# Kernel tuning notes

Measured on AMD Instinct MI355X. Metric: run time of the kernel, lower is better.

The kernel has to match this reference:

```python
import jax, jax.numpy as jnp
import numpy as np

SEQ_LEN, BATCH, TAGS = 512, 1024, 32
START_IDX, END_IDX = 30, 31
NEG = -10000.0


def setup_inputs() -> dict:
    key = jax.random.key(0)
    k1, k2 = jax.random.split(key)
    feats = jax.random.normal(k1, (SEQ_LEN, BATCH, TAGS), dtype=jnp.float32)
    mask = jnp.ones((SEQ_LEN, BATCH), dtype=jnp.float32)
    # xavier-normal-ish transition, then apply START/END constraints as in reset_parameters
    transition = jax.random.normal(k2, (TAGS, TAGS), dtype=jnp.float32) * (2.0 / (TAGS + TAGS)) ** 0.5
    transition = transition.at[START_IDX, :].set(NEG)
    transition = transition.at[:, END_IDX].set(NEG)
    return {"feats": feats, "mask": mask, "transition": transition}


def reference(feats, mask, transition):
    # feats: (T, N, M), mask: (T, N), transition: (M, M)
    batch_size, tag_size = feats.shape[1], feats.shape[2]
    alpha0 = jnp.full((batch_size, tag_size), NEG, dtype=feats.dtype)
    alpha0 = alpha0.at[:, START_IDX].set(0.0)

    def step(alpha, inp):
        feat_t, mask_t = inp  # (N, M), (N,)
        # score[n, j, i] = alpha[n, i] + transition[j, i] + feat[n, j]
        score = alpha[:, None, :] + transition[None, :, :] + feat_t[:, :, None]
        new_alpha = jax.nn.logsumexp(score, axis=-1)  # (N, M)
        m = mask_t[:, None]
        alpha = new_alpha * m + alpha * (1.0 - m)
        return alpha, None

    alpha, _ = jax.lax.scan(step, alpha0, (feats, mask))
    alpha = alpha + transition[END_IDX][None, :]
    return jax.nn.logsumexp(alpha, axis=-1)  # (N,)
```

## Files before the change

### kernel.cpp

```cpp
#include <hip/hip_runtime.h>


constexpr int SEQ = 512, BATCH = 1024, TAGS = 32;
constexpr int NC = 8, L = SEQ / NC;
constexpr int RROW = 16;

#define LOG2E 1.4426950408889634f
#define LN2   0.6931471805599453f

typedef __attribute__((ext_vector_type(8))) short short8;
typedef __attribute__((ext_vector_type(4))) float float4v;
typedef __attribute__((ext_vector_type(4))) unsigned uint4v;
union Frag8 { unsigned u[4]; short8 v; };

__device__ __forceinline__ unsigned pk_rn(float x, float y) {
  return __builtin_amdgcn_perm(__float_as_uint(y) + 0x8000u,
                               __float_as_uint(x) + 0x8000u, 0x07060302u);
}
__device__ __forceinline__ unsigned pk_tr(float x, float y) {
  return __builtin_amdgcn_perm(__float_as_uint(y), __float_as_uint(x), 0x07060302u);
}

extern "C" __global__ void __launch_bounds__(512, 6) crf_fused(
    const float* __restrict__ feats, const float* __restrict__ mask,
    const float* __restrict__ trans, float* __restrict__ out) {
  __shared__ unsigned gst[NC][66 * RROW];
  __shared__ float c2s[NC];
  __shared__ __align__(16) float ws[TAGS];
  __shared__ float c2x;

  const int wid = __builtin_amdgcn_readfirstlane((int)(threadIdx.x >> 6));
  const int lane = threadIdx.x & 63;
  const int b = blockIdx.x;
  const int s = lane & 15, q = lane >> 4;
  unsigned* Wp = &gst[wid][0];

  unsigned long long mb;
  {
    const float* fro = feats + ((size_t)(wid * L + lane) * BATCH + b) * TAGS;
    float4v fv[8];
#pragma unroll
    for (int i = 0; i < 8; ++i) fv[i] = *(const float4v*)(fro + 4 * i);
    const float mv = mask[(size_t)(wid * L + lane) * BATCH + b];
    mb = __ballot(mv != 0.0f);
    unsigned* rp = Wp + lane * RROW;
#pragma unroll
    for (int g = 0; g < 4; ++g) {
      uint4v t;
#pragma unroll
      for (int k2 = 0; k2 < 4; ++k2) {
        const int j = 4 * g + k2;
        const float lo = __builtin_amdgcn_exp2f(fv[j >> 2][j & 3] * LOG2E);
        const float hi = __builtin_amdgcn_exp2f(fv[4 + (j >> 2)][j & 3] * LOG2E);
        t[k2] = pk_rn(lo, hi);
      }
      *(uint4v*)(rp + 4 * g) = t;
    }
  }

  int sig[8];
#pragma unroll
  for (int i = 0; i < 8; ++i) sig[i] = (i < 4) ? (4 * q + i) : (16 + 4 * q + (i - 4));
  Frag8 e0, e1;
#pragma unroll
  for (int p = 0; p < 4; ++p) {
    e0.u[p] = pk_rn(__builtin_amdgcn_exp2f(trans[s * TAGS + sig[2 * p]] * LOG2E),
                    __builtin_amdgcn_exp2f(trans[s * TAGS + sig[2 * p + 1]] * LOG2E));
    e1.u[p] = pk_rn(__builtin_amdgcn_exp2f(trans[(16 + s) * TAGS + sig[2 * p]] * LOG2E),
                    __builtin_amdgcn_exp2f(trans[(16 + s) * TAGS + sig[2 * p + 1]] * LOG2E));
  }

  float4v P00 = {0, 0, 0, 0}, P01 = {0, 0, 0, 0}, P10 = {0, 0, 0, 0}, P11 = {0, 0, 0, 0};
#pragma unroll
  for (int p = 0; p < 4; ++p) {
    float one = (4 * q + p == s) ? 1.f : 0.f;
    P00[p] = one; P11[p] = one;
  }
  Frag8 B0, B1;
  float c2 = 0.f;
  const float4v zerov = {0.f, 0.f, 0.f, 0.f};

#define PACK_B()                                                        \
  { B0.u[0] = pk_tr(P00[0], P00[1]); B0.u[1] = pk_tr(P00[2], P00[3]);   \
    B0.u[2] = pk_tr(P10[0], P10[1]); B0.u[3] = pk_tr(P10[2], P10[3]);   \
    B1.u[0] = pk_tr(P01[0], P01[1]); B1.u[1] = pk_tr(P01[2], P01[3]);   \
    B1.u[2] = pk_tr(P11[0], P11[1]); B1.u[3] = pk_tr(P11[2], P11[3]); }
  PACK_B()

#define RDU(t) (*(const uint4v*)(Wp + (t) * RROW + 4 * q))

  uint4v Ua = RDU(0), Ub = RDU(1);

#pragma unroll 8
  for (int r = 0; r < L; ++r) {
    const uint4v U = (r & 1) ? Ub : Ua;
    if (r & 1) Ub = RDU(r + 2); else Ua = RDU(r + 2);

    if ((mb >> r) & 1ull) {
      float4v F0, F1;
#pragma unroll
      for (int i = 0; i < 4; ++i) {
        F0[i] = __uint_as_float(U[i] << 16);
        F1[i] = __uint_as_float(U[i] & 0xffff0000u);
      }
      float4v D00 = __builtin_amdgcn_mfma_f32_16x16x32_bf16(e0.v, B0.v, zerov, 0, 0, 0);
      float4v D01 = __builtin_amdgcn_mfma_f32_16x16x32_bf16(e0.v, B1.v, zerov, 0, 0, 0);
      float4v D10 = __builtin_amdgcn_mfma_f32_16x16x32_bf16(e1.v, B0.v, zerov, 0, 0, 0);
      float4v D11 = __builtin_amdgcn_mfma_f32_16x16x32_bf16(e1.v, B1.v, zerov, 0, 0, 0);
      P00 = D00 * F0; P01 = D01 * F0;
      P10 = D10 * F1; P11 = D11 * F1;
      PACK_B()
    }

    if ((r & 7) == 7) {
      float4v m4 = __builtin_elementwise_max(__builtin_elementwise_max(P00, P01),
                                             __builtin_elementwise_max(P10, P11));
      float mx = fmaxf(fmaxf(m4[0], m4[1]), fmaxf(m4[2], m4[3]));
      mx = fmaxf(mx, __shfl_xor(mx, 1, 64));
      mx = fmaxf(mx, __shfl_xor(mx, 2, 64));
      mx = fmaxf(mx, __shfl_xor(mx, 4, 64));
      mx = fmaxf(mx, __shfl_xor(mx, 8, 64));
      mx = fmaxf(mx, __shfl_xor(mx, 16, 64));
      mx = fmaxf(mx, __shfl_xor(mx, 32, 64));
      int ex = (int)((__float_as_uint(mx) >> 23) & 0xFFu) - 127;
      float scl = __uint_as_float((unsigned)(127 - ex) << 23);
      P00 *= scl; P01 *= scl; P10 *= scl; P11 *= scl;
      c2 += (float)ex;
      PACK_B()
    }
  }

  if (lane == 0) c2s[wid] = c2;
  if (threadIdx.x == 0) c2x = 0.f;
  __syncthreads();

  for (int k = NC - 1; k >= 0; --k) {
    if (wid == k) {
      float4v w0, w1;
      if (k == NC - 1) {
#pragma unroll
        for (int p = 0; p < 4; ++p) {
          w0[p] = __builtin_amdgcn_exp2f(trans[31 * TAGS + 4 * q + p] * LOG2E);
          w1[p] = __builtin_amdgcn_exp2f(trans[31 * TAGS + 16 + 4 * q + p] * LOG2E);
        }
      } else {
        w0 = *(const float4v*)(ws + 4 * q);
        w1 = *(const float4v*)(ws + 16 + 4 * q);
      }
      float ps = 0.f, pt = 0.f;
#pragma unroll
      for (int p = 0; p < 4; ++p) {
        ps += w0[p] * P00[p] + w1[p] * P10[p];
        pt += w0[p] * P01[p] + w1[p] * P11[p];
      }
      ps += __shfl_xor(ps, 16, 64); ps += __shfl_xor(ps, 32, 64);
      pt += __shfl_xor(pt, 16, 64); pt += __shfl_xor(pt, 32, 64);
      if (k > 0) {
        float mx = fmaxf(ps, pt);
        mx = fmaxf(mx, __shfl_xor(mx, 1, 64));
        mx = fmaxf(mx, __shfl_xor(mx, 2, 64));
        mx = fmaxf(mx, __shfl_xor(mx, 4, 64));
        mx = fmaxf(mx, __shfl_xor(mx, 8, 64));
        int ex = (int)((__float_as_uint(mx) >> 23) & 0xFFu) - 127;
        float scl = __uint_as_float((unsigned)(127 - ex) << 23);
        ps *= scl; pt *= scl;
        if (lane == 0) c2x += (float)ex;
        if (lane < 16) { ws[lane] = ps; ws[16 + lane] = pt; }
      } else if (lane == 14) {
        float c2t = ((c2s[0] + c2s[1]) + (c2s[2] + c2s[3])) +
                    ((c2s[4] + c2s[5]) + (c2s[6] + c2s[7])) + c2x;
        out[b] = LN2 * (c2t + __builtin_amdgcn_logf(pt));
      }
    }
    __syncthreads();
  }
}

extern "C" void kernel_launch(void* const* d_in, const int* in_sizes, int n_in,
                              void* d_out, int out_size, void* d_ws, size_t ws_size,
                              hipStream_t stream) {
  const float* feats = (const float*)d_in[0];
  const float* mask  = (const float*)d_in[1];
  const float* trans = (const float*)d_in[2];
  float* out = (float*)d_out;
  hipLaunchKernelGGL(crf_fused, dim3(BATCH), dim3(512), 0, stream,
                     feats, mask, trans, out);
}
```

Measured before the change: 131.2 us.

## Interleave two independent half-chunk chains per wave to hide MFMA latency

```diff
diff --git a/kernel.cpp b/kernel.cpp
--- a/kernel.cpp
+++ b/kernel.cpp
@@ -2,7 +2,8 @@
 
 
 constexpr int SEQ = 512, BATCH = 1024, TAGS = 32;
-constexpr int NC = 8, L = SEQ / NC;
+constexpr int NW = 8;
+constexpr int LH = 32;
 constexpr int RROW = 16;
 
 #define LOG2E 1.4426950408889634f
@@ -21,11 +22,11 @@
   return __builtin_amdgcn_perm(__float_as_uint(y), __float_as_uint(x), 0x07060302u);
 }
 
-extern "C" __global__ void __launch_bounds__(512, 6) crf_fused(
+extern "C" __global__ void __launch_bounds__(512, 4) crf_fused(
     const float* __restrict__ feats, const float* __restrict__ mask,
     const float* __restrict__ trans, float* __restrict__ out) {
-  __shared__ unsigned gst[NC][66 * RROW];
-  __shared__ float c2s[NC];
+  __shared__ unsigned gst[NW][66 * RROW];
+  __shared__ float c2s[NW];
   __shared__ __align__(16) float ws[TAGS];
   __shared__ float c2x;
 
@@ -37,11 +38,11 @@
 
   unsigned long long mb;
   {
-    const float* fro = feats + ((size_t)(wid * L + lane) * BATCH + b) * TAGS;
+    const float* fro = feats + ((size_t)(wid * 64 + lane) * BATCH + b) * TAGS;
     float4v fv[8];
 #pragma unroll
     for (int i = 0; i < 8; ++i) fv[i] = *(const float4v*)(fro + 4 * i);
-    const float mv = mask[(size_t)(wid * L + lane) * BATCH + b];
+    const float mv = mask[(size_t)(wid * 64 + lane) * BATCH + b];
     mb = __ballot(mv != 0.0f);
     unsigned* rp = Wp + lane * RROW;
 #pragma unroll
@@ -70,74 +71,88 @@
                     __builtin_amdgcn_exp2f(trans[(16 + s) * TAGS + sig[2 * p + 1]] * LOG2E));
   }
 
-  float4v P00 = {0, 0, 0, 0}, P01 = {0, 0, 0, 0}, P10 = {0, 0, 0, 0}, P11 = {0, 0, 0, 0};
+  float4v PX00 = {0,0,0,0}, PX01 = {0,0,0,0}, PX10 = {0,0,0,0}, PX11 = {0,0,0,0};
+  float4v PY00 = {0,0,0,0}, PY01 = {0,0,0,0}, PY10 = {0,0,0,0}, PY11 = {0,0,0,0};
 #pragma unroll
   for (int p = 0; p < 4; ++p) {
     float one = (4 * q + p == s) ? 1.f : 0.f;
-    P00[p] = one; P11[p] = one;
-  }
-  Frag8 B0, B1;
-  float c2 = 0.f;
+    PX00[p] = one; PX11[p] = one; PY00[p] = one; PY11[p] = one;
+  }
+  Frag8 BX0, BX1, BY0, BY1;
+  float c2X = 0.f, c2Y = 0.f;
   const float4v zerov = {0.f, 0.f, 0.f, 0.f};
 
-#define PACK_B()                                                        \
+#define PACK_B(B0, B1, P00, P01, P10, P11)                              \
   { B0.u[0] = pk_tr(P00[0], P00[1]); B0.u[1] = pk_tr(P00[2], P00[3]);   \
     B0.u[2] = pk_tr(P10[0], P10[1]); B0.u[3] = pk_tr(P10[2], P10[3]);   \
     B1.u[0] = pk_tr(P01[0], P01[1]); B1.u[1] = pk_tr(P01[2], P01[3]);   \
     B1.u[2] = pk_tr(P11[0], P11[1]); B1.u[3] = pk_tr(P11[2], P11[3]); }
-  PACK_B()
+
+  PACK_B(BX0, BX1, PX00, PX01, PX10, PX11)
+  PACK_B(BY0, BY1, PY00, PY01, PY10, PY11)
+
+#define STEP(U, B0, B1, P00, P01, P10, P11)                             \
+  { float4v F0, F1;                                                     \
+    _Pragma("unroll")                                                   \
+    for (int i = 0; i < 4; ++i) {                                       \
+      F0[i] = __uint_as_float(U[i] << 16);                              \
+      F1[i] = __uint_as_float(U[i] & 0xffff0000u);                      \
+    }                                                                   \
+    float4v D00 = __builtin_amdgcn_mfma_f32_16x16x32_bf16(e0.v, B0.v, zerov, 0, 0, 0); \
+    float4v D01 = __builtin_amdgcn_mfma_f32_16x16x32_bf16(e0.v, B1.v, zerov, 0, 0, 0); \
+    float4v D10 = __builtin_amdgcn_mfma_f32_16x16x32_bf16(e1.v, B0.v, zerov, 0, 0, 0); \
+    float4v D11 = __builtin_amdgcn_mfma_f32_16x16x32_bf16(e1.v, B1.v, zerov, 0, 0, 0); \
+    P00 = D00 * F0; P01 = D01 * F0;                                     \
+    P10 = D10 * F1; P11 = D11 * F1;                                     \
+    PACK_B(B0, B1, P00, P01, P10, P11) }
+
+#define RENORM(P00, P01, P10, P11, B0, B1, C2)                          \
+  { float4v m4 = __builtin_elementwise_max(__builtin_elementwise_max(P00, P01), \
+                                           __builtin_elementwise_max(P10, P11)); \
+    float mx = fmaxf(fmaxf(m4[0], m4[1]), fmaxf(m4[2], m4[3]));         \
+    mx = fmaxf(mx, __shfl_xor(mx, 1, 64));                              \
+    mx = fmaxf(mx, __shfl_xor(mx, 2, 64));                              \
+    mx = fmaxf(mx, __shfl_xor(mx, 4, 64));                              \
+    mx = fmaxf(mx, __shfl_xor(mx, 8, 64));                              \
+    mx = fmaxf(mx, __shfl_xor(mx, 16, 64));                             \
+    mx = fmaxf(mx, __shfl_xor(mx, 32, 64));                             \
+    int ex = (int)((__float_as_uint(mx) >> 23) & 0xFFu) - 127;          \
+    float scl = __uint_as_float((unsigned)(127 - ex) << 23);            \
+    P00 *= scl; P01 *= scl; P10 *= scl; P11 *= scl;                     \
+    C2 += (float)ex;                                                    \
+    PACK_B(B0, B1, P00, P01, P10, P11) }
 
 #define RDU(t) (*(const uint4v*)(Wp + (t) * RROW + 4 * q))
 
-  uint4v Ua = RDU(0), Ub = RDU(1);
+  uint4v UX = RDU(0), UY = RDU(32);
 
 #pragma unroll 8
-  for (int r = 0; r < L; ++r) {
-    const uint4v U = (r & 1) ? Ub : Ua;
-    if (r & 1) Ub = RDU(r + 2); else Ua = RDU(r + 2);
-
-    if ((mb >> r) & 1ull) {
-      float4v F0, F1;
-#pragma unroll
-      for (int i = 0; i < 4; ++i) {
-        F0[i] = __uint_as_float(U[i] << 16);
-        F1[i] = __uint_as_float(U[i] & 0xffff0000u);
-      }
-      float4v D00 = __builtin_amdgcn_mfma_f32_16x16x32_bf16(e0.v, B0.v, zerov, 0, 0, 0);
-      float4v D01 = __builtin_amdgcn_mfma_f32_16x16x32_bf16(e0.v, B1.v, zerov, 0, 0, 0);
-      float4v D10 = __builtin_amdgcn_mfma_f32_16x16x32_bf16(e1.v, B0.v, zerov, 0, 0, 0);
-      float4v D11 = __builtin_amdgcn_mfma_f32_16x16x32_bf16(e1.v, B1.v, zerov, 0, 0, 0);
-      P00 = D00 * F0; P01 = D01 * F0;
-      P10 = D10 * F1; P11 = D11 * F1;
-      PACK_B()
-    }
-
+  for (int r = 0; r < LH; ++r) {
+    uint4v UXn = RDU(r + 1), UYn = RDU(33 + r);
+    const bool bx = (mb >> r) & 1ull;
+    const bool by = (mb >> (32 + r)) & 1ull;
+    if (bx & by) {
+      STEP(UX, BX0, BX1, PX00, PX01, PX10, PX11)
+      STEP(UY, BY0, BY1, PY00, PY01, PY10, PY11)
+    } else {
+      if (bx) STEP(UX, BX0, BX1, PX00, PX01, PX10, PX11)
+      if (by) STEP(UY, BY0, BY1, PY00, PY01, PY10, PY11)
+    }
     if ((r & 7) == 7) {
-      float4v m4 = __builtin_elementwise_max(__builtin_elementwise_max(P00, P01),
-                                             __builtin_elementwise_max(P10, P11));
-      float mx = fmaxf(fmaxf(m4[0], m4[1]), fmaxf(m4[2], m4[3]));
-      mx = fmaxf(mx, __shfl_xor(mx, 1, 64));
-      mx = fmaxf(mx, __shfl_xor(mx, 2, 64));
-      mx = fmaxf(mx, __shfl_xor(mx, 4, 64));
-      mx = fmaxf(mx, __shfl_xor(mx, 8, 64));
-      mx = fmaxf(mx, __shfl_xor(mx, 16, 64));
-      mx = fmaxf(mx, __shfl_xor(mx, 32, 64));
-      int ex = (int)((__float_as_uint(mx) >> 23) & 0xFFu) - 127;
-      float scl = __uint_as_float((unsigned)(127 - ex) << 23);
-      P00 *= scl; P01 *= scl; P10 *= scl; P11 *= scl;
-      c2 += (float)ex;
-      PACK_B()
-    }
-  }
-
-  if (lane == 0) c2s[wid] = c2;
+      RENORM(PX00, PX01, PX10, PX11, BX0, BX1, c2X)
+      RENORM(PY00, PY01, PY10, PY11, BY0, BY1, c2Y)
+    }
+    UX = UXn; UY = UYn;
+  }
+
+  if (lane == 0) c2s[wid] = c2X + c2Y;
   if (threadIdx.x == 0) c2x = 0.f;
   __syncthreads();
 
-  for (int k = NC - 1; k >= 0; --k) {
+  for (int k = NW - 1; k >= 0; --k) {
     if (wid == k) {
       float4v w0, w1;
-      if (k == NC - 1) {
+      if (k == NW - 1) {
 #pragma unroll
         for (int p = 0; p < 4; ++p) {
           w0[p] = __builtin_amdgcn_exp2f(trans[31 * TAGS + 4 * q + p] * LOG2E);
@@ -150,8 +165,21 @@
       float ps = 0.f, pt = 0.f;
 #pragma unroll
       for (int p = 0; p < 4; ++p) {
-        ps += w0[p] * P00[p] + w1[p] * P10[p];
-        pt += w0[p] * P01[p] + w1[p] * P11[p];
+        ps += w0[p] * PY00[p] + w1[p] * PY10[p];
+        pt += w0[p] * PY01[p] + w1[p] * PY11[p];
+      }
+      ps += __shfl_xor(ps, 16, 64); ps += __shfl_xor(ps, 32, 64);
+      pt += __shfl_xor(pt, 16, 64); pt += __shfl_xor(pt, 32, 64);
+#pragma unroll
+      for (int p = 0; p < 4; ++p) {
+        w0[p] = __shfl(ps, 4 * q + p, 64);
+        w1[p] = __shfl(pt, 4 * q + p, 64);
+      }
+      ps = 0.f; pt = 0.f;
+#pragma unroll
+      for (int p = 0; p < 4; ++p) {
+        ps += w0[p] * PX00[p] + w1[p] * PX10[p];
+        pt += w0[p] * PX01[p] + w1[p] * PX11[p];
       }
       ps += __shfl_xor(ps, 16, 64); ps += __shfl_xor(ps, 32, 64);
       pt += __shfl_xor(pt, 16, 64); pt += __shfl_xor(pt, 32, 64);
```

New measurement: 139.3 us. 1.06x slower.
